# Kernel optimization log

Measured on AMD Instinct MI355X. Metric: run time of the kernel, lower is better.

The kernel has to match this reference:

```python
import jax, jax.numpy as jnp
import numpy as np

B, QN, KVN = 4, 512, 512
QD, KD, H, VD = 512, 512, 256, 256


def setup_inputs() -> dict:
    key = jax.random.key(0)
    ks = jax.random.split(key, 6)
    q = jax.random.normal(ks[0], (B, QN, QD), dtype=jnp.float32)
    k = jax.random.normal(ks[1], (B, KVN, KD), dtype=jnp.float32)
    v = jax.random.normal(ks[2], (B, KVN, VD), dtype=jnp.float32)
    # Linear weights (torch nn.Linear stores [out, in]; bias=False)
    Wq = jax.random.normal(ks[3], (H, QD), dtype=jnp.float32) / np.sqrt(QD)
    Wk = jax.random.normal(ks[4], (H, KD), dtype=jnp.float32) / np.sqrt(KD)
    wv = jax.random.normal(ks[5], (H,), dtype=jnp.float32) / np.sqrt(H)
    return {"q": q, "k": k, "v": v, "Wq": Wq, "Wk": Wk, "wv": wv}


def reference(q, k, v, Wq, Wk, wv):
    # Project queries and keys to hidden dim H
    qh = jnp.einsum("bqd,hd->bqh", q, Wq)  # [B, QN, H]
    kh = jnp.einsum("bkd,hd->bkh", k, Wk)  # [B, KVN, H]
    # Broadcast add + tanh: [B, QN, KVN, H]
    energy = jnp.tanh(qh[:, :, None, :] + kh[:, None, :, :])
    # Score projection to scalar per (q, kv) pair
    scores = jnp.einsum("bqkh,h->bqk", energy, wv)  # [B, QN, KVN]
    attention = jax.nn.softmax(scores, axis=-1)
    # Dropout omitted (inference mode)
    output = jnp.einsum("bqk,bkv->bqv", attention, v)  # [B, QN, VD]
    return (output, attention)
```

## Files before the change

### kernel.cpp

```cpp
#include <hip/hip_runtime.h>

#define B_ 4
#define QN 512
#define KVN 512
#define QD_ 512
#define H_ 256
#define VD_ 256
#define TOTR 2048

typedef __attribute__((ext_vector_type(8))) short bf16x8;
typedef __attribute__((ext_vector_type(4))) float f32x4;
typedef __attribute__((ext_vector_type(4))) unsigned short u16x4;
typedef unsigned short u16;

__device__ __forceinline__ float rcp_(float x) { return __builtin_amdgcn_rcpf(x); }
__device__ __forceinline__ float ex2_(float x) { return __builtin_amdgcn_exp2f(x); }

__device__ __forceinline__ u16 bf16_rne(float x) {
    unsigned u = __float_as_uint(x);
    unsigned r = u + 0x7FFFu + ((u >> 16) & 1u);
    return (u16)(r >> 16);
}
__device__ __forceinline__ void split2(float x, u16& h, u16& l) {
    h = bf16_rne(x);
    float hf = __uint_as_float((unsigned)h << 16);
    l = bf16_rne(x - hf);
}
__device__ __forceinline__ void split4(float4 a, u16x4& h, u16x4& l) {
    u16 hh, ll;
    split2(a.x, hh, ll); h[0] = hh; l[0] = ll;
    split2(a.y, hh, ll); h[1] = hh; l[1] = ll;
    split2(a.z, hh, ll); h[2] = hh; l[2] = ll;
    split2(a.w, hh, ll); h[3] = hh; l[3] = ll;
}

__global__ __launch_bounds__(256) void prep(const float* __restrict__ q,
                                            const float* __restrict__ k,
                                            const float* __restrict__ Wq,
                                            const float* __restrict__ Wk,
                                            const float* __restrict__ v,
                                            u16* __restrict__ q_hi, u16* __restrict__ q_lo,
                                            u16* __restrict__ k_hi, u16* __restrict__ k_lo,
                                            u16* __restrict__ w_hi, u16* __restrict__ w_lo,
                                            u16* __restrict__ vt_hi, u16* __restrict__ vt_lo) {
    __shared__ float ts[64][65];
    const int tid = threadIdx.x;
    if (blockIdx.x < 2304) {
        const int NQ = 2048 * 512 / 4, NW = 256 * 512 / 4;
        int idx = blockIdx.x * 256 + tid;
        const float* src; u16 *dh, *dl; int off;
        if (idx < NQ)               { src = q;  dh = q_hi; dl = q_lo; off = idx; }
        else if (idx < 2 * NQ)      { src = k;  dh = k_hi; dl = k_lo; off = idx - NQ; }
        else if (idx < 2 * NQ + NW) { src = Wq; dh = w_hi; dl = w_lo; off = idx - 2 * NQ; }
        else { src = Wk; dh = w_hi + 256 * 512; dl = w_lo + 256 * 512; off = idx - 2 * NQ - NW; }
        float4 v4 = ((const float4*)src)[off];
        u16x4 h, l;
        split4(v4, h, l);
        *(u16x4*)(dh + off * 4) = h;
        *(u16x4*)(dl + off * 4) = l;
    } else {
        int bid = blockIdx.x - 2304;
        int j0 = (bid & 7) * 64, n0 = ((bid >> 3) & 3) * 64, b = bid >> 5;
#pragma unroll
        for (int t = 0; t < 4; ++t) {
            int idx = t * 256 + tid;
            int j = idx >> 4, nq = idx & 15;
            float4 v4 = *(const float4*)(v + ((size_t)b * KVN + j0 + j) * VD_ + n0 + nq * 4);
            *(float4*)&ts[j][nq * 4] = v4;
        }
        __syncthreads();
#pragma unroll
        for (int t = 0; t < 4; ++t) {
            int idx = t * 256 + tid;
            int jq = idx & 15, n = idx >> 4;
            u16x4 h, l;
            u16 hh, ll;
#pragma unroll
            for (int e = 0; e < 4; ++e) {
                split2(ts[jq * 4 + e][n], hh, ll);
                h[e] = hh; l[e] = ll;
            }
            size_t off = ((size_t)b * VD_ + n0 + n) * KVN + j0 + jq * 4;
            *(u16x4*)(vt_hi + off) = h;
            *(u16x4*)(vt_lo + off) = l;
        }
    }
}

__global__ __launch_bounds__(256) void proj_mfma(const u16* __restrict__ q_hi, const u16* __restrict__ q_lo,
                                                 const u16* __restrict__ k_hi, const u16* __restrict__ k_lo,
                                                 const u16* __restrict__ w_hi, const u16* __restrict__ w_lo,
                                                 float* __restrict__ eq, float* __restrict__ ekT) {
    const int z = blockIdx.z;
    const u16* __restrict__ Ah_g = z ? k_hi : q_hi;
    const u16* __restrict__ Al_g = z ? k_lo : q_lo;
    const u16* __restrict__ Bh_g = w_hi + (size_t)z * H_ * QD_;
    const u16* __restrict__ Bl_g = w_lo + (size_t)z * H_ * QD_;
    __shared__ u16 Ash[4][32][8], Asl[4][32][8], Bsh[4][32][8], Bsl[4][32][8];
    const int tid = threadIdx.x;
    const int wave = tid >> 6, lane = tid & 63;
    const int fl = lane & 15, kg = lane >> 4;
    const int r0 = blockIdx.y * 32, c0 = blockIdx.x * 32;
    const int ar = 16 * (wave & 1), bc = 16 * (wave >> 1);
    const int frow = (tid & 127) >> 2, fkq = tid & 3, fsel = tid >> 7;
    f32x4 acc = {};
    for (int k0 = 0; k0 < QD_; k0 += 32) {
        __syncthreads();
        {
            const u16* as = (fsel ? Al_g : Ah_g) + (size_t)(r0 + frow) * QD_ + k0 + fkq * 8;
            u16* ad = fsel ? &Asl[fkq][frow][0] : &Ash[fkq][frow][0];
            *(uint4*)ad = *(const uint4*)as;
            const u16* bs = (fsel ? Bl_g : Bh_g) + (size_t)(c0 + frow) * QD_ + k0 + fkq * 8;
            u16* bd = fsel ? &Bsl[fkq][frow][0] : &Bsh[fkq][frow][0];
            *(uint4*)bd = *(const uint4*)bs;
        }
        __syncthreads();
        bf16x8 a_h = *(const bf16x8*)&Ash[kg][ar + fl][0];
        bf16x8 a_l = *(const bf16x8*)&Asl[kg][ar + fl][0];
        bf16x8 b_h = *(const bf16x8*)&Bsh[kg][bc + fl][0];
        bf16x8 b_l = *(const bf16x8*)&Bsl[kg][bc + fl][0];
        acc = __builtin_amdgcn_mfma_f32_16x16x32_bf16(a_h, b_h, acc, 0, 0, 0);
        acc = __builtin_amdgcn_mfma_f32_16x16x32_bf16(a_h, b_l, acc, 0, 0, 0);
        acc = __builtin_amdgcn_mfma_f32_16x16x32_bf16(a_l, b_h, acc, 0, 0, 0);
    }
    const float cs = 2.8853900817779268f;
    const int rg = kg * 4;
    if (z == 1) {
        float4 o = {ex2_(acc[0] * cs), ex2_(acc[1] * cs), ex2_(acc[2] * cs), ex2_(acc[3] * cs)};
        *(float4*)(ekT + (size_t)(c0 + bc + fl) * TOTR + r0 + ar + rg) = o;
    } else {
#pragma unroll
        for (int r = 0; r < 4; ++r)
            eq[(size_t)(r0 + ar + rg + r) * H_ + c0 + bc + fl] = ex2_(acc[r] * cs);
    }
}

__global__ __launch_bounds__(256, 8) void scores_v6(const float* __restrict__ eq,
                                                    const float* __restrict__ ekT,
                                                    const float* __restrict__ wv,
                                                    float* __restrict__ scpart) {
    const int tid = threadIdx.x;
    const int wid = tid >> 6, lane = tid & 63;
    const int hs = blockIdx.z;
    const int h0 = hs * 32;
    const int row0 = blockIdx.y * 32;
    const int b = row0 >> 9;
    const int jloc = blockIdx.x * 256 + wid * 64 + lane;
    const int colg = b * KVN + jloc;

    float ekr[32];
#pragma unroll
    for (int hh = 0; hh < 32; ++hh)
        ekr[hh] = ekT[(size_t)(h0 + hh) * TOTR + colg];

    float4 wr[8];
#pragma unroll
    for (int g = 0; g < 8; ++g) wr[g] = *(const float4*)(wv + h0 + g * 4);

    const float* __restrict__ eqrow = eq + (size_t)row0 * H_ + h0;
    float* __restrict__ outp = scpart + (size_t)hs * TOTR * KVN + (size_t)row0 * KVN + jloc;

#pragma unroll 4
    for (int qq = 0; qq < 32; ++qq) {
        const float* ep = eqrow + (size_t)qq * H_;
        float s = 0.f;
#pragma unroll
        for (int g = 0; g < 8; ++g) {
            float4 e = *(const float4*)(ep + 4 * g);
            float a  = __builtin_fmaf(ekr[4 * g + 0], e.x, 1.0f);
            float bb = __builtin_fmaf(ekr[4 * g + 1], e.y, 1.0f);
            float cc = __builtin_fmaf(ekr[4 * g + 2], e.z, 1.0f);
            float dd = __builtin_fmaf(ekr[4 * g + 3], e.w, 1.0f);
            float ab = a * bb, cd = cc * dd;
            float n1 = __builtin_fmaf(wr[g].y, a, wr[g].x * bb);
            float n2 = __builtin_fmaf(wr[g].w, cc, wr[g].z * dd);
            float num = __builtin_fmaf(n2, ab, n1 * cd);
            s = __builtin_fmaf(num, rcp_(ab * cd), s);
        }
        outp[(size_t)qq * KVN] = -2.0f * s;
    }
}

__global__ __launch_bounds__(256) void softmax2(const float* __restrict__ scpart,
                                                float* __restrict__ attn,
                                                u16* __restrict__ at_hi,
                                                u16* __restrict__ at_lo) {
    const size_t PS = (size_t)TOTR * KVN;
    int row = blockIdx.x;
    int tid = threadIdx.x;
    const float* p = scpart + (size_t)row * KVN;
    float x0 = 0.f, x1 = 0.f;
#pragma unroll
    for (int hsplit = 0; hsplit < 8; ++hsplit) {
        x0 += p[hsplit * PS + tid];
        x1 += p[hsplit * PS + tid + 256];
    }
    float e0 = __expf(x0), e1 = __expf(x1);
    float s = e0 + e1;
#pragma unroll
    for (int d = 1; d < 64; d <<= 1) s += __shfl_xor(s, d);
    __shared__ float reds[4];
    int wave = tid >> 6, lane = tid & 63;
    if (lane == 0) reds[wave] = s;
    __syncthreads();
    s = reds[0] + reds[1] + reds[2] + reds[3];
    float inv = rcp_(s);
    float r0v = e0 * inv, r1v = e1 * inv;
    float* o = attn + (size_t)row * KVN;
    o[tid] = r0v;
    o[tid + 256] = r1v;
    u16 h, l;
    size_t base = (size_t)row * KVN;
    split2(r0v, h, l);
    at_hi[base + tid] = h; at_lo[base + tid] = l;
    split2(r1v, h, l);
    at_hi[base + tid + 256] = h; at_lo[base + tid + 256] = l;
}

__global__ __launch_bounds__(256) void out_mfma(const u16* __restrict__ vt_hi, const u16* __restrict__ vt_lo,
                                                const u16* __restrict__ at_hi, const u16* __restrict__ at_lo,
                                                float* __restrict__ out) {
    const int b = blockIdx.z;
    const u16* __restrict__ Ah_g = vt_hi + (size_t)b * VD_ * KVN;
    const u16* __restrict__ Al_g = vt_lo + (size_t)b * VD_ * KVN;
    const u16* __restrict__ Bh_g = at_hi + (size_t)b * QN * KVN;
    const u16* __restrict__ Bl_g = at_lo + (size_t)b * QN * KVN;
    float* __restrict__ outb = out + (size_t)b * QN * VD_;
    __shared__ u16 Ash[4][32][8], Asl[4][32][8], Bsh[4][32][8], Bsl[4][32][8];
    const int tid = threadIdx.x;
    const int wave = tid >> 6, lane = tid & 63;
    const int fl = lane & 15, kg = lane >> 4;
    const int r0 = blockIdx.y * 32;
    const int c0 = blockIdx.x * 32;
    const int ar = 16 * (wave & 1), bc = 16 * (wave >> 1);
    const int frow = (tid & 127) >> 2, fkq = tid & 3, fsel = tid >> 7;
    f32x4 acc = {};
    for (int k0 = 0; k0 < KVN; k0 += 32) {
        __syncthreads();
        {
            const u16* as = (fsel ? Al_g : Ah_g) + (size_t)(r0 + frow) * KVN + k0 + fkq * 8;
            u16* ad = fsel ? &Asl[fkq][frow][0] : &Ash[fkq][frow][0];
            *(uint4*)ad = *(const uint4*)as;
            const u16* bs = (fsel ? Bl_g : Bh_g) + (size_t)(c0 + frow) * KVN + k0 + fkq * 8;
            u16* bd = fsel ? &Bsl[fkq][frow][0] : &Bsh[fkq][frow][0];
            *(uint4*)bd = *(const uint4*)bs;
        }
        __syncthreads();
        bf16x8 a_h = *(const bf16x8*)&Ash[kg][ar + fl][0];
        bf16x8 a_l = *(const bf16x8*)&Asl[kg][ar + fl][0];
        bf16x8 b_h = *(const bf16x8*)&Bsh[kg][bc + fl][0];
        bf16x8 b_l = *(const bf16x8*)&Bsl[kg][bc + fl][0];
        acc = __builtin_amdgcn_mfma_f32_16x16x32_bf16(a_h, b_h, acc, 0, 0, 0);
        acc = __builtin_amdgcn_mfma_f32_16x16x32_bf16(a_h, b_l, acc, 0, 0, 0);
        acc = __builtin_amdgcn_mfma_f32_16x16x32_bf16(a_l, b_h, acc, 0, 0, 0);
    }
    const int rg = kg * 4;
    float4 o = {acc[0], acc[1], acc[2], acc[3]};
    *(float4*)(outb + (size_t)(c0 + bc + fl) * VD_ + r0 + ar + rg) = o;
}

extern "C" void kernel_launch(void* const* d_in, const int* in_sizes, int n_in,
                              void* d_out, int out_size, void* d_ws, size_t ws_size,
                              hipStream_t stream) {
    const float* q  = (const float*)d_in[0];
    const float* k  = (const float*)d_in[1];
    const float* v  = (const float*)d_in[2];
    const float* Wq = (const float*)d_in[3];
    const float* Wk = (const float*)d_in[4];
    const float* wv = (const float*)d_in[5];
    float* out  = (float*)d_out;
    float* attn = out + (size_t)B_ * QN * VD_;

    float* eq  = (float*)d_ws;
    float* ekT = eq + (size_t)TOTR * H_;
    u16* q_hi = (u16*)(ekT + (size_t)H_ * TOTR);
    u16* q_lo = q_hi + 2048 * 512;
    u16* k_hi = q_lo + 2048 * 512;
    u16* k_lo = k_hi + 2048 * 512;
    u16* w_hi = k_lo + 2048 * 512;
    u16* w_lo = w_hi + 512 * 512;
    u16* vt_hi = w_lo + 512 * 512;
    u16* vt_lo = vt_hi + (size_t)B_ * VD_ * KVN;
    float* scpart = (float*)(vt_lo + (size_t)B_ * VD_ * KVN);
    u16* at_hi = q_hi;
    u16* at_lo = q_lo;

    prep<<<2432, 256, 0, stream>>>(q, k, Wq, Wk, v, q_hi, q_lo, k_hi, k_lo,
                                   w_hi, w_lo, vt_hi, vt_lo);
    proj_mfma<<<dim3(H_ / 32, 2048 / 32, 2), 256, 0, stream>>>(q_hi, q_lo, k_hi, k_lo,
                                                               w_hi, w_lo, eq, ekT);
    scores_v6<<<dim3(2, TOTR / 32, 8), 256, 0, stream>>>(eq, ekT, wv, scpart);
    softmax2<<<TOTR, 256, 0, stream>>>(scpart, attn, at_hi, at_lo);
    out_mfma<<<dim3(QN / 32, VD_ / 32, B_), 256, 0, stream>>>(vt_hi, vt_lo, at_hi, at_lo, out);
}
```

Before: 83.17 us.

## Fold wv reciprocal into eq projection and simplify tanh-sum algebra in scores

The exp(2qh) projection output is pre-divided by wv in the projection epilogue. The scores kernel can then compute each wv*tanh term as a pairwise (d0+d1)/(d0*d1) sum with fewer multiplies and one reciprocal per pair. The -2 scale and the constant offset (which cancels in softmax) move into softmax2. The scores tile is also halved to 16 rows with launch bounds lowered to 4 blocks per SM, doubling the grid. Risks: dividing by wv values near zero could overflow or lose precision, and the extra iwv registers may affect occupancy.

Measured after the change: 74.43 us. 10.5% less time.

```diff
diff --git a/kernel.cpp b/kernel.cpp
--- a/kernel.cpp
+++ b/kernel.cpp
@@ -90,7 +90,8 @@
 __global__ __launch_bounds__(256) void proj_mfma(const u16* __restrict__ q_hi, const u16* __restrict__ q_lo,
                                                  const u16* __restrict__ k_hi, const u16* __restrict__ k_lo,
                                                  const u16* __restrict__ w_hi, const u16* __restrict__ w_lo,
-                                                 float* __restrict__ eq, float* __restrict__ ekT) {
+                                                 const float* __restrict__ wv,
+                                                 float* __restrict__ eqw, float* __restrict__ ekT) {
     const int z = blockIdx.z;
     const u16* __restrict__ Ah_g = z ? k_hi : q_hi;
     const u16* __restrict__ Al_g = z ? k_lo : q_lo;
@@ -129,13 +130,14 @@
         float4 o = {ex2_(acc[0] * cs), ex2_(acc[1] * cs), ex2_(acc[2] * cs), ex2_(acc[3] * cs)};
         *(float4*)(ekT + (size_t)(c0 + bc + fl) * TOTR + r0 + ar + rg) = o;
     } else {
+        float iw = rcp_(wv[c0 + bc + fl]);
 #pragma unroll
         for (int r = 0; r < 4; ++r)
-            eq[(size_t)(r0 + ar + rg + r) * H_ + c0 + bc + fl] = ex2_(acc[r] * cs);
-    }
-}
-
-__global__ __launch_bounds__(256, 8) void scores_v6(const float* __restrict__ eq,
+            eqw[(size_t)(r0 + ar + rg + r) * H_ + c0 + bc + fl] = ex2_(acc[r] * cs) * iw;
+    }
+}
+
+__global__ __launch_bounds__(256, 4) void scores_v7(const float* __restrict__ eqw,
                                                     const float* __restrict__ ekT,
                                                     const float* __restrict__ wv,
                                                     float* __restrict__ scpart) {
@@ -143,41 +145,42 @@
     const int wid = tid >> 6, lane = tid & 63;
     const int hs = blockIdx.z;
     const int h0 = hs * 32;
-    const int row0 = blockIdx.y * 32;
+    const int row0 = blockIdx.y * 16;
     const int b = row0 >> 9;
     const int jloc = blockIdx.x * 256 + wid * 64 + lane;
     const int colg = b * KVN + jloc;
 
-    float ekr[32];
+    float ekr[32], iwv[32];
 #pragma unroll
     for (int hh = 0; hh < 32; ++hh)
         ekr[hh] = ekT[(size_t)(h0 + hh) * TOTR + colg];
-
-    float4 wr[8];
-#pragma unroll
-    for (int g = 0; g < 8; ++g) wr[g] = *(const float4*)(wv + h0 + g * 4);
-
-    const float* __restrict__ eqrow = eq + (size_t)row0 * H_ + h0;
+#pragma unroll
+    for (int g = 0; g < 8; ++g) {
+        float4 w4 = *(const float4*)(wv + h0 + 4 * g);
+        iwv[4 * g + 0] = rcp_(w4.x);
+        iwv[4 * g + 1] = rcp_(w4.y);
+        iwv[4 * g + 2] = rcp_(w4.z);
+        iwv[4 * g + 3] = rcp_(w4.w);
+    }
+
+    const float* __restrict__ eqrow = eqw + (size_t)row0 * H_ + h0;
     float* __restrict__ outp = scpart + (size_t)hs * TOTR * KVN + (size_t)row0 * KVN + jloc;
 
-#pragma unroll 4
-    for (int qq = 0; qq < 32; ++qq) {
+#pragma unroll 2
+    for (int qq = 0; qq < 16; ++qq) {
         const float* ep = eqrow + (size_t)qq * H_;
         float s = 0.f;
 #pragma unroll
         for (int g = 0; g < 8; ++g) {
             float4 e = *(const float4*)(ep + 4 * g);
-            float a  = __builtin_fmaf(ekr[4 * g + 0], e.x, 1.0f);
-            float bb = __builtin_fmaf(ekr[4 * g + 1], e.y, 1.0f);
-            float cc = __builtin_fmaf(ekr[4 * g + 2], e.z, 1.0f);
-            float dd = __builtin_fmaf(ekr[4 * g + 3], e.w, 1.0f);
-            float ab = a * bb, cd = cc * dd;
-            float n1 = __builtin_fmaf(wr[g].y, a, wr[g].x * bb);
-            float n2 = __builtin_fmaf(wr[g].w, cc, wr[g].z * dd);
-            float num = __builtin_fmaf(n2, ab, n1 * cd);
-            s = __builtin_fmaf(num, rcp_(ab * cd), s);
-        }
-        outp[(size_t)qq * KVN] = -2.0f * s;
+            float d0 = __builtin_fmaf(ekr[4 * g + 0], e.x, iwv[4 * g + 0]);
+            float d1 = __builtin_fmaf(ekr[4 * g + 1], e.y, iwv[4 * g + 1]);
+            float d2 = __builtin_fmaf(ekr[4 * g + 2], e.z, iwv[4 * g + 2]);
+            float d3 = __builtin_fmaf(ekr[4 * g + 3], e.w, iwv[4 * g + 3]);
+            s = __builtin_fmaf(d0 + d1, rcp_(d0 * d1), s);
+            s = __builtin_fmaf(d2 + d3, rcp_(d2 * d3), s);
+        }
+        outp[(size_t)qq * KVN] = s;
     }
 }
 
@@ -195,7 +198,7 @@
         x0 += p[hsplit * PS + tid];
         x1 += p[hsplit * PS + tid + 256];
     }
-    float e0 = __expf(x0), e1 = __expf(x1);
+    float e0 = __expf(-2.0f * x0), e1 = __expf(-2.0f * x1);
     float s = e0 + e1;
 #pragma unroll
     for (int d = 1; d < 64; d <<= 1) s += __shfl_xor(s, d);
@@ -271,8 +274,8 @@
     float* out  = (float*)d_out;
     float* attn = out + (size_t)B_ * QN * VD_;
 
-    float* eq  = (float*)d_ws;
-    float* ekT = eq + (size_t)TOTR * H_;
+    float* eqw = (float*)d_ws;
+    float* ekT = eqw + (size_t)TOTR * H_;
     u16* q_hi = (u16*)(ekT + (size_t)H_ * TOTR);
     u16* q_lo = q_hi + 2048 * 512;
     u16* k_hi = q_lo + 2048 * 512;
@@ -288,8 +291,8 @@
     prep<<<2432, 256, 0, stream>>>(q, k, Wq, Wk, v, q_hi, q_lo, k_hi, k_lo,
                                    w_hi, w_lo, vt_hi, vt_lo);
     proj_mfma<<<dim3(H_ / 32, 2048 / 32, 2), 256, 0, stream>>>(q_hi, q_lo, k_hi, k_lo,
-                                                               w_hi, w_lo, eq, ekT);
-    scores_v6<<<dim3(2, TOTR / 32, 8), 256, 0, stream>>>(eq, ekT, wv, scpart);
+                                                               w_hi, w_lo, wv, eqw, ekT);
+    scores_v7<<<dim3(2, TOTR / 16, 8), 256, 0, stream>>>(eqw, ekT, wv, scpart);
     softmax2<<<TOTR, 256, 0, stream>>>(scpart, attn, at_hi, at_lo);
     out_mfma<<<dim3(QN / 32, VD_ / 32, B_), 256, 0, stream>>>(vt_hi, vt_lo, at_hi, at_lo, out);
 }
```
